# Performance work log

Measured on AMD Instinct MI355X. Metric: run time of the kernel, lower is better.

## Reference

```python
import jax, jax.numpy as jnp
import numpy as np

N, E = 50000, 800000
IN_C, OUT_C, HEADS = 256, 64, 4
NEG_SLOPE = 0.2


def setup_inputs() -> dict:
    key = jax.random.key(0)
    k1, k2, k3, k4, k5, k6 = jax.random.split(key, 6)
    x = jax.random.normal(k1, (N, IN_C), dtype=jnp.float32)
    edge_index = jax.random.randint(k2, (2, E), 0, N, dtype=jnp.int64)
    # Glorot-style init for parameters
    W = jax.random.normal(k3, (IN_C, HEADS * OUT_C), dtype=jnp.float32) * (1.0 / np.sqrt(IN_C))
    att_src = jax.random.normal(k4, (HEADS, OUT_C), dtype=jnp.float32) * (1.0 / np.sqrt(OUT_C))
    att_dst = jax.random.normal(k5, (HEADS, OUT_C), dtype=jnp.float32) * (1.0 / np.sqrt(OUT_C))
    bias = jnp.zeros((HEADS * OUT_C,), dtype=jnp.float32)
    return {"x": x, "edge_index": edge_index, "W": W,
            "att_src": att_src, "att_dst": att_dst, "bias": bias}


def reference(x, edge_index, W, att_src, att_dst, bias):
    n = x.shape[0]
    # add self loops (PyG GATConv default add_self_loops=True)
    loops = jnp.arange(n, dtype=edge_index.dtype)
    src = jnp.concatenate([edge_index[0], loops])  # [E+N]
    dst = jnp.concatenate([edge_index[1], loops])  # [E+N]

    h = (x @ W).reshape(n, HEADS, OUT_C)  # [N, H, C]
    a_src = jnp.einsum('nhc,hc->nh', h, att_src)  # [N, H]
    a_dst = jnp.einsum('nhc,hc->nh', h, att_dst)  # [N, H]

    # per-edge attention logits with leaky relu
    alpha = a_src[src] + a_dst[dst]  # [E+N, H]
    alpha = jnp.where(alpha >= 0, alpha, NEG_SLOPE * alpha)

    # segment softmax over destination nodes
    amax = jax.ops.segment_max(alpha, dst, num_segments=n)  # [N, H]
    amax = jax.lax.stop_gradient(jnp.where(jnp.isfinite(amax), amax, 0.0))
    ex = jnp.exp(alpha - amax[dst])  # [E+N, H]
    denom = jax.ops.segment_sum(ex, dst, num_segments=n)  # [N, H]
    coef = ex / (denom[dst] + 1e-16)  # [E+N, H]

    # weighted scatter-add aggregation of source features
    msgs = h[src] * coef[:, :, None]  # [E+N, H, C]
    out = jax.ops.segment_sum(msgs, dst, num_segments=n)  # [N, H, C]
    return out.reshape(n, HEADS * OUT_C) + bias
```

## Files before the change

kernel.cpp:

```cpp
#include <hip/hip_runtime.h>
#include <hip/hip_bf16.h>

#define HEADS 4
#define OUT_C 64
#define CH 256
#define NEG_SLOPE 0.2f
#define CAP 64

typedef short short8 __attribute__((ext_vector_type(8)));
typedef float f32x4 __attribute__((ext_vector_type(4)));

__device__ inline float bflo(unsigned int u) {
    return __uint_as_float(u << 16);
}
__device__ inline float bfhi(unsigned int u) {
    return __uint_as_float(u & 0xFFFF0000u);
}
__device__ inline unsigned short f2bf(float f) {
    __hip_bfloat16 b = __float2bfloat16(f);
    return *reinterpret_cast<unsigned short*>(&b);
}

#define GLOAD_LDS16(g, l)                                                   \
    __builtin_amdgcn_global_load_lds(                                       \
        (const __attribute__((address_space(1))) void*)(g),                 \
        (__attribute__((address_space(3))) void*)(l), 16, 0, 0)

__global__ __launch_bounds__(256) void init_kernel(int* __restrict__ cnt,
                                                   const float* __restrict__ W,
                                                   unsigned short* __restrict__ wt,
                                                   int N, int ZB) {
    int b = blockIdx.x;
    if (b < ZB) {
        int i = b * 256 + threadIdx.x;
        if (i < N) cnt[i] = 0;
    } else {
        int n = b - ZB;
        int k = threadIdx.x;
        wt[n * 256 + k] = f2bf(W[k * 256 + n]);
    }
}

__global__ __launch_bounds__(256) void gemm_scatter_kernel(
        const float* __restrict__ x,
        const unsigned short* __restrict__ wt,
        const float* __restrict__ att_src,
        const float* __restrict__ att_dst,
        unsigned short* __restrict__ h16,
        float* __restrict__ a_src,
        float* __restrict__ a_dst,
        int M,
        const int* __restrict__ ei,
        int* __restrict__ cnt,
        int* __restrict__ srclist,
        int E, int GB, int SCB) {
    __shared__ float As[64 * 64];
    __shared__ unsigned short Bs[256 * 64];

    int stripe = blockIdx.x / 9, r9 = blockIdx.x % 9;
    int tid = threadIdx.x;

    if (r9 >= 4) {
        int sb = stripe * 5 + (r9 - 4);
        if (sb >= SCB) return;
        int i = sb * 256 + tid;
        int E4 = E >> 2;
        if (i < E4) {
            int4 s4 = ((const int4*)ei)[i];
            int4 d4 = ((const int4*)(ei + E))[i];
            if ((unsigned)s4.x < (unsigned)M && (unsigned)d4.x < (unsigned)M) {
                int idx = atomicAdd(&cnt[d4.x], 1);
                if (idx < CAP) srclist[(d4.x << 6) + idx] = s4.x;
            }
            if ((unsigned)s4.y < (unsigned)M && (unsigned)d4.y < (unsigned)M) {
                int idx = atomicAdd(&cnt[d4.y], 1);
                if (idx < CAP) srclist[(d4.y << 6) + idx] = s4.y;
            }
            if ((unsigned)s4.z < (unsigned)M && (unsigned)d4.z < (unsigned)M) {
                int idx = atomicAdd(&cnt[d4.z], 1);
                if (idx < CAP) srclist[(d4.z << 6) + idx] = s4.z;
            }
            if ((unsigned)s4.w < (unsigned)M && (unsigned)d4.w < (unsigned)M) {
                int idx = atomicAdd(&cnt[d4.w], 1);
                if (idx < CAP) srclist[(d4.w << 6) + idx] = s4.w;
            }
        } else if (i < E4 + M) {
            int n = i - E4;
            int idx = atomicAdd(&cnt[n], 1);
            if (idx < CAP) srclist[(n << 6) + idx] = n;
        }
        return;
    }

    int gid = stripe * 4 + r9;
    if (gid >= GB) return;

    int w = tid >> 6, l = tid & 63;
    int wr = w >> 1, wc = w & 1;
    int quad = l >> 4, m16 = l & 15;
    int row0 = gid * 64;

    f32x4 acc[2][8];
    #pragma unroll
    for (int t = 0; t < 2; ++t)
        #pragma unroll
        for (int u = 0; u < 8; ++u) acc[t][u] = (f32x4)(0.f);

    const float4* As4 = (const float4*)As;

    for (int k0 = 0; k0 < CH; k0 += 64) {
        #pragma unroll
        for (int q = 0; q < 4; ++q) {
            int cslot = q * 256 + tid;
            int rr = cslot >> 4, cs = cslot & 15;
            int j = cs ^ (rr & 15);
            int grow = row0 + rr; if (grow > M - 1) grow = M - 1;
            const float* gp = x + (size_t)grow * CH + k0 + j * 4;
            GLOAD_LDS16(gp, As + cslot * 4);
        }
        #pragma unroll
        for (int q = 0; q < 8; ++q) {
            int cslot = q * 256 + tid;
            int rr = cslot >> 3, cs = cslot & 7;
            int j = cs ^ (rr & 7);
            const unsigned short* gp = wt + (size_t)rr * CH + k0 + j * 8;
            GLOAD_LDS16(gp, Bs + cslot * 8);
        }
        __syncthreads();
        #pragma unroll
        for (int ks = 0; ks < 2; ++ks) {
            int jj = ks * 4 + quad;
            short8 af[2], bf[8];
            #pragma unroll
            for (int t = 0; t < 2; ++t) {
                int ra = wr * 32 + t * 16 + m16;
                float4 f0 = As4[ra * 16 + ((jj * 2)     ^ (ra & 15))];
                float4 f1 = As4[ra * 16 + ((jj * 2 + 1) ^ (ra & 15))];
                short8 v;
                v[0] = (short)f2bf(f0.x); v[1] = (short)f2bf(f0.y);
                v[2] = (short)f2bf(f0.z); v[3] = (short)f2bf(f0.w);
                v[4] = (short)f2bf(f1.x); v[5] = (short)f2bf(f1.y);
                v[6] = (short)f2bf(f1.z); v[7] = (short)f2bf(f1.w);
                af[t] = v;
            }
            #pragma unroll
            for (int u = 0; u < 8; ++u) {
                int c = wc * 128 + u * 16 + m16;
                int cs = jj ^ (c & 7);
                bf[u] = *reinterpret_cast<const short8*>(Bs + (c * 8 + cs) * 8);
            }
            #pragma unroll
            for (int t = 0; t < 2; ++t)
                #pragma unroll
                for (int u = 0; u < 8; ++u)
                    acc[t][u] = __builtin_amdgcn_mfma_f32_16x16x32_bf16(
                        af[t], bf[u], acc[t][u], 0, 0, 0);
        }
        __syncthreads();
    }

    float asr[8], adr[8];
    #pragma unroll
    for (int u = 0; u < 8; ++u) {
        int c = wc * 128 + u * 16 + m16;
        asr[u] = att_src[c];
        adr[u] = att_dst[c];
    }

    #pragma unroll
    for (int t = 0; t < 2; ++t) {
        #pragma unroll
        for (int reg = 0; reg < 4; ++reg) {
            int row = row0 + wr * 32 + t * 16 + quad * 4 + reg;
            float sv0 = 0.f, sv1 = 0.f, dv0 = 0.f, dv1 = 0.f;
            #pragma unroll
            for (int u = 0; u < 4; ++u) {
                float c0 = acc[t][u][reg];
                float c1 = acc[t][u + 4][reg];
                sv0 += c0 * asr[u];     dv0 += c0 * adr[u];
                sv1 += c1 * asr[u + 4]; dv1 += c1 * adr[u + 4];
            }
            #pragma unroll
            for (int o = 8; o > 0; o >>= 1) {
                sv0 += __shfl_xor(sv0, o, 64);
                sv1 += __shfl_xor(sv1, o, 64);
                dv0 += __shfl_xor(dv0, o, 64);
                dv1 += __shfl_xor(dv1, o, 64);
            }
            if (row < M) {
                #pragma unroll
                for (int u = 0; u < 8; ++u)
                    h16[(size_t)row * CH + wc * 128 + u * 16 + m16] =
                        f2bf(acc[t][u][reg]);
                if (m16 == 0) {
                    float2 s2 = {sv0, sv1};
                    float2 d2 = {dv0, dv1};
                    *(float2*)(a_src + row * HEADS + wc * 2) = s2;
                    *(float2*)(a_dst + row * HEADS + wc * 2) = d2;
                }
            }
        }
    }
}

__global__ __launch_bounds__(256) void aggregate_kernel(const unsigned short* __restrict__ h16,
                                                        const float4* __restrict__ a_src4,
                                                        const float4* __restrict__ a_dst4,
                                                        const int* __restrict__ cnt,
                                                        const int* __restrict__ srclist,
                                                        const float* __restrict__ bias,
                                                        float* __restrict__ out,
                                                        int N) {
    int tid = threadIdx.x;
    int w = tid >> 6, lane = tid & 63;
    int half = lane >> 5, l32 = lane & 31;
    int headC = l32 >> 3;
    int g = lane >> 2;
    int headS = lane & 3;
    int n = blockIdx.x * 4 + w;
    if (n >= N) return;

    int c = cnt[n]; if (c > CAP) c = CAP;
    int start = n << 6;
    float4 ad = a_dst4[n];
    float adS = headS == 0 ? ad.x : headS == 1 ? ad.y : headS == 2 ? ad.z : ad.w;

    float facc[8];
    #pragma unroll
    for (int j = 0; j < 8; ++j) facc[j] = 0.f;
    float denom = 0.f;

    for (int base = 0; base < c; base += 16) {
        int cntc = min(c - base, 16);
        int sg = (g < cntc) ? srclist[start + base + g] : 0;
        float4 a = a_src4[sg];
        float av = headS == 0 ? a.x : headS == 1 ? a.y : headS == 2 ? a.z : a.w;
        float al = av + adS;
        al = (al >= 0.f) ? al : NEG_SLOPE * al;
        float ew = __expf(al);
        #pragma unroll
        for (int j = 0; j < 8; ++j) {
            int i = half * 8 + j;
            if (i < cntc) {
                int s   = __shfl(sg, i * 4, 64);
                float e = __shfl(ew, i * 4 + headC, 64);
                uint4 u = *((const uint4*)(h16 + (size_t)s * CH) + l32);
                denom += e;
                facc[0] += e * bflo(u.x);
                facc[1] += e * bfhi(u.x);
                facc[2] += e * bflo(u.y);
                facc[3] += e * bfhi(u.y);
                facc[4] += e * bflo(u.z);
                facc[5] += e * bfhi(u.z);
                facc[6] += e * bflo(u.w);
                facc[7] += e * bfhi(u.w);
            }
        }
    }

    #pragma unroll
    for (int j = 0; j < 8; ++j) facc[j] += __shfl_xor(facc[j], 32, 64);
    denom += __shfl_xor(denom, 32, 64);

    float inv = 1.f / (denom + 1e-16f);
    int cbase = l32 * 8 + half * 4;
    float4 b4 = *(const float4*)(bias + cbase);
    f32x4 o4;
    o4[0] = (half ? facc[4] : facc[0]) * inv + b4.x;
    o4[1] = (half ? facc[5] : facc[1]) * inv + b4.y;
    o4[2] = (half ? facc[6] : facc[2]) * inv + b4.z;
    o4[3] = (half ? facc[7] : facc[3]) * inv + b4.w;
    __builtin_nontemporal_store(o4, (f32x4*)(out + (size_t)n * CH + cbase));
}

extern "C" void kernel_launch(void* const* d_in, const int* in_sizes, int n_in,
                              void* d_out, int out_size, void* d_ws, size_t ws_size,
                              hipStream_t stream) {
    const float* x       = (const float*)d_in[0];
    const int*   ei      = (const int*)d_in[1];
    const float* W       = (const float*)d_in[2];
    const float* att_src = (const float*)d_in[3];
    const float* att_dst = (const float*)d_in[4];
    const float* bias    = (const float*)d_in[5];
    float* out = (float*)d_out;

    int N = in_sizes[0] / CH;
    int E = in_sizes[1] / 2;

    auto align = [](size_t v) { return (v + 255) & ~(size_t)255; };
    char* ws = (char*)d_ws;
    size_t off = 0;
    unsigned short* h16 = (unsigned short*)(ws + off); off = align(off + (size_t)N * CH * 2);
    unsigned short* wt  = (unsigned short*)(ws + off); off = align(off + (size_t)CH * CH * 2);
    float* a_src  = (float*)(ws + off); off = align(off + (size_t)N * HEADS * 4);
    float* a_dst  = (float*)(ws + off); off = align(off + (size_t)N * HEADS * 4);
    int*   cnt    = (int*)(ws + off);   off = align(off + (size_t)N * 4);
    int*   srclist= (int*)(ws + off);   off = align(off + (size_t)N * CAP * 4);

    int ZB = (N + 255) / 256;
    init_kernel<<<ZB + 256, 256, 0, stream>>>(cnt, W, wt, N, ZB);

    int E4 = E / 4;
    int GB  = (N + 63) / 64;
    int SCB = (E4 + N + 255) / 256;
    int ns_g = (GB + 3) / 4, ns_s = (SCB + 4) / 5;
    int NST = ns_g > ns_s ? ns_g : ns_s;
    gemm_scatter_kernel<<<NST * 9, 256, 0, stream>>>(x, wt, att_src, att_dst,
                                                     h16, a_src, a_dst, N,
                                                     ei, cnt, srclist, E, GB, SCB);

    aggregate_kernel<<<(N + 3) / 4, 256, 0, stream>>>(h16, (const float4*)a_src,
                                                      (const float4*)a_dst,
                                                      cnt, srclist, bias, out, N);
}
```

Measured before the change: 219.9 us.

## Double-buffer GEMM K-tiles in LDS to overlap global loads with MFMA

The GEMM main loop now uses two LDS buffers with a K-step of 32 instead of a single buffer with K-step 64. The next tile is issued via global_load_lds while the current one is consumed, using manual vmcnt waits and raw barriers. This is meant to hide global load latency behind MFMA work. In exchange there are more loop iterations and barriers, and correctness depends on the hand-counted vmcnt(6) matching the six loads issued per stage.

Measured after the change: 227.1 us. 1.03x slower.

```diff
diff --git a/kernel.cpp b/kernel.cpp
--- a/kernel.cpp
+++ b/kernel.cpp
@@ -54,8 +54,8 @@
         int* __restrict__ cnt,
         int* __restrict__ srclist,
         int E, int GB, int SCB) {
-    __shared__ float As[64 * 64];
-    __shared__ unsigned short Bs[256 * 64];
+    __shared__ float As[2][64 * 32];
+    __shared__ unsigned short Bs[2][256 * 32];
 
     int stripe = blockIdx.x / 9, r9 = blockIdx.x % 9;
     int tid = threadIdx.x;
@@ -106,58 +106,71 @@
         #pragma unroll
         for (int u = 0; u < 8; ++u) acc[t][u] = (f32x4)(0.f);
 
-    const float4* As4 = (const float4*)As;
-
-    for (int k0 = 0; k0 < CH; k0 += 64) {
+    auto stage = [&](int bsel, int k0) {
+        #pragma unroll
+        for (int q = 0; q < 2; ++q) {
+            int cslot = q * 256 + tid;
+            int r = cslot >> 3, cs = cslot & 7;
+            int j = cs ^ (r & 7);
+            int grow = row0 + r; if (grow > M - 1) grow = M - 1;
+            const float* gp = x + (size_t)grow * CH + k0 + j * 4;
+            GLOAD_LDS16(gp, &As[bsel][cslot * 4]);
+        }
         #pragma unroll
         for (int q = 0; q < 4; ++q) {
             int cslot = q * 256 + tid;
-            int rr = cslot >> 4, cs = cslot & 15;
-            int j = cs ^ (rr & 15);
-            int grow = row0 + rr; if (grow > M - 1) grow = M - 1;
-            const float* gp = x + (size_t)grow * CH + k0 + j * 4;
-            GLOAD_LDS16(gp, As + cslot * 4);
-        }
-        #pragma unroll
-        for (int q = 0; q < 8; ++q) {
-            int cslot = q * 256 + tid;
-            int rr = cslot >> 3, cs = cslot & 7;
-            int j = cs ^ (rr & 7);
-            const unsigned short* gp = wt + (size_t)rr * CH + k0 + j * 8;
-            GLOAD_LDS16(gp, Bs + cslot * 8);
-        }
-        __syncthreads();
-        #pragma unroll
-        for (int ks = 0; ks < 2; ++ks) {
-            int jj = ks * 4 + quad;
-            short8 af[2], bf[8];
+            int r = cslot >> 2, cs = cslot & 3;
+            int j = cs ^ (r & 3);
+            const unsigned short* gp = wt + (size_t)r * CH + k0 + j * 8;
+            GLOAD_LDS16(gp, &Bs[bsel][cslot * 8]);
+        }
+    };
+
+    auto compute = [&](int bsel) {
+        const float4* A4 = (const float4*)As[bsel];
+        short8 af[2], bf[8];
+        #pragma unroll
+        for (int t = 0; t < 2; ++t) {
+            int r = wr * 32 + t * 16 + m16;
+            float4 f0 = A4[r * 8 + ((2 * quad)     ^ (r & 7))];
+            float4 f1 = A4[r * 8 + ((2 * quad + 1) ^ (r & 7))];
+            short8 v;
+            v[0] = (short)f2bf(f0.x); v[1] = (short)f2bf(f0.y);
+            v[2] = (short)f2bf(f0.z); v[3] = (short)f2bf(f0.w);
+            v[4] = (short)f2bf(f1.x); v[5] = (short)f2bf(f1.y);
+            v[6] = (short)f2bf(f1.z); v[7] = (short)f2bf(f1.w);
+            af[t] = v;
+        }
+        #pragma unroll
+        for (int u = 0; u < 8; ++u) {
+            int c = wc * 128 + u * 16 + m16;
+            bf[u] = *reinterpret_cast<const short8*>(
+                &Bs[bsel][(c * 4 + (quad ^ (c & 3))) * 8]);
+        }
+        #pragma unroll
+        for (int t = 0; t < 2; ++t)
             #pragma unroll
-            for (int t = 0; t < 2; ++t) {
-                int ra = wr * 32 + t * 16 + m16;
-                float4 f0 = As4[ra * 16 + ((jj * 2)     ^ (ra & 15))];
-                float4 f1 = As4[ra * 16 + ((jj * 2 + 1) ^ (ra & 15))];
-                short8 v;
-                v[0] = (short)f2bf(f0.x); v[1] = (short)f2bf(f0.y);
-                v[2] = (short)f2bf(f0.z); v[3] = (short)f2bf(f0.w);
-                v[4] = (short)f2bf(f1.x); v[5] = (short)f2bf(f1.y);
-                v[6] = (short)f2bf(f1.z); v[7] = (short)f2bf(f1.w);
-                af[t] = v;
-            }
-            #pragma unroll
-            for (int u = 0; u < 8; ++u) {
-                int c = wc * 128 + u * 16 + m16;
-                int cs = jj ^ (c & 7);
-                bf[u] = *reinterpret_cast<const short8*>(Bs + (c * 8 + cs) * 8);
-            }
-            #pragma unroll
-            for (int t = 0; t < 2; ++t)
-                #pragma unroll
-                for (int u = 0; u < 8; ++u)
-                    acc[t][u] = __builtin_amdgcn_mfma_f32_16x16x32_bf16(
-                        af[t], bf[u], acc[t][u], 0, 0, 0);
-        }
-        __syncthreads();
-    }
+            for (int u = 0; u < 8; ++u)
+                acc[t][u] = __builtin_amdgcn_mfma_f32_16x16x32_bf16(
+                    af[t], bf[u], acc[t][u], 0, 0, 0);
+    };
+
+    stage(0, 0);
+    int b = 0;
+    for (int step = 0; step < 7; ++step) {
+        stage(b ^ 1, (step + 1) * 32);
+        asm volatile("s_waitcnt vmcnt(6)" ::: "memory");
+        __builtin_amdgcn_s_barrier();
+        __builtin_amdgcn_sched_barrier(0);
+        compute(b);
+        asm volatile("s_waitcnt lgkmcnt(0)" ::: "memory");
+        __builtin_amdgcn_s_barrier();
+        b ^= 1;
+    }
+    asm volatile("s_waitcnt vmcnt(0)" ::: "memory");
+    __builtin_amdgcn_s_barrier();
+    __builtin_amdgcn_sched_barrier(0);
+    compute(b);
 
     float asr[8], adr[8];
     #pragma unroll
```
